# Performance work log

Hardware: AMD Instinct MI355X
Metric: run time of the kernel (lower is better)

Reference implementation:

```python
import jax, jax.numpy as jnp
import numpy as np

LEVELS = 2
_H0 = jnp.array([0.0322231, -0.01260397, -0.09921954, 0.2978578,
                 0.80373875, 0.49761867, -0.02963553, -0.07576571], dtype=jnp.float32)
_H1 = _H0[::-1] * jnp.array([-1.0, 1.0] * 4, dtype=jnp.float32)  # db4 QMF


def subband_conv2d(x, kernel_2d, stride):
    # depthwise grouped conv: same 2D kernel applied to every channel
    C = x.shape[-1]
    k = jnp.tile(kernel_2d[:, :, None, None], (1, 1, 1, C))  # HWIO with I=1, groups=C
    return jax.lax.conv_general_dilated(
        x, k, window_strides=(stride, stride), padding='SAME',
        dimension_numbers=('NHWC', 'HWIO', 'NHWC'), feature_group_count=C)


def _upsample2d(t):
    B, H, W, C = t.shape
    return jnp.zeros((B, 2 * H, 2 * W, C), t.dtype).at[:, ::2, ::2, :].set(t)


def _local_conv(t, w):
    # per-spatial-position linear map over channels: [B,H,W,I] x [I,O,W,H] -> [B,H,W,O]
    return jnp.einsum('bhwi,iowh->bhwo', t, w)


def setup_inputs() -> dict:
    key = jax.random.key(0)
    ks = jax.random.split(key, 9)
    B, H, W, C, O = 16, 128, 128, 64, 64
    inp = {
        'x': jax.random.normal(ks[0], (B, H, W, C), dtype=jnp.float32),
        'wLL': 0.02 * jax.random.normal(ks[1], (C, O, 32, 32), dtype=jnp.float32),
        'wLH_l0': 0.02 * jax.random.normal(ks[2], (C, O, 64, 64), dtype=jnp.float32),
        'wHL_l0': 0.02 * jax.random.normal(ks[3], (C, O, 64, 64), dtype=jnp.float32),
        'wHH_l0': 0.02 * jax.random.normal(ks[4], (C, O, 64, 64), dtype=jnp.float32),
        'wLH_l1': 0.02 * jax.random.normal(ks[5], (C, O, 32, 32), dtype=jnp.float32),
        'wHL_l1': 0.02 * jax.random.normal(ks[6], (C, O, 32, 32), dtype=jnp.float32),
        'wHH_l1': 0.02 * jax.random.normal(ks[7], (C, O, 32, 32), dtype=jnp.float32),
    }
    return inp


def reference(x, wLL, wLH_l0, wHL_l0, wHH_l0, wLH_l1, wHL_l1, wHH_l1):
    h0, h1 = _H0, _H1
    g0, g1 = h0[::-1], h1[::-1]
    # H=W=128 is divisible by 2**levels, so no symmetric padding is needed.
    res = x
    details = []
    for _ in range(LEVELS):
        cLL = subband_conv2d(res, jnp.outer(h0, h0), 2)
        cLH = subband_conv2d(res, jnp.outer(h0, h1), 2)
        cHL = subband_conv2d(res, jnp.outer(h1, h0), 2)
        cHH = subband_conv2d(res, jnp.outer(h1, h1), 2)
        details.append((cLH, cHL, cHH))
        res = cLL
    yA = _local_conv(res, wLL)  # [B,32,32,O]
    det_w = [(wLH_l0, wHL_l0, wHH_l0), (wLH_l1, wHL_l1, wHH_l1)]
    td = []
    for i in range(LEVELS):
        lh, hl, hh = details[i]
        wlh, whl, whh = det_w[i]
        td.append((_local_conv(lh, wlh), _local_conv(hl, whl), _local_conv(hh, whh)))
    r = yA
    for i in reversed(range(LEVELS)):
        yLH, yHL, yHH = td[i]
        r = (subband_conv2d(_upsample2d(r), jnp.outer(g0, g0), 1)
             + subband_conv2d(_upsample2d(yLH), jnp.outer(g0, g1), 1)
             + subband_conv2d(_upsample2d(yHL), jnp.outer(g1, g0), 1)
             + subband_conv2d(_upsample2d(yHH), jnp.outer(g1, g1), 1))
    return r
```

## Files before the change

kernel.cpp:

```cpp
#include <hip/hip_runtime.h>

__device__ __constant__ float H0[8] = { 0.0322231f, -0.01260397f, -0.09921954f,  0.2978578f,
                                        0.80373875f, 0.49761867f, -0.02963553f, -0.07576571f};
__device__ __constant__ float H1[8] = { 0.07576571f, -0.02963553f, -0.49761867f, 0.80373875f,
                                       -0.2978578f, -0.09921954f,  0.01260397f,  0.0322231f};
__device__ __constant__ float G0[8] = {-0.07576571f, -0.02963553f,  0.49761867f, 0.80373875f,
                                        0.2978578f,  -0.09921954f, -0.01260397f, 0.0322231f};
__device__ __constant__ float G1[8] = { 0.0322231f,   0.01260397f, -0.09921954f, -0.2978578f,
                                        0.80373875f, -0.49761867f, -0.02963553f, 0.07576571f};

template<int HIN>
__global__ __launch_bounds__(256) void fwd_dwt(const float* __restrict__ in,
                                               float* __restrict__ oLL, float* __restrict__ oLH,
                                               float* __restrict__ oHL, float* __restrict__ oHH)
{
    constexpr int OH = HIN / 2;
    constexpr int TQ = OH / 2;
    const int tid = threadIdx.x;
    const int c = tid & 63;
    const int s = blockIdx.x * 4 + (tid >> 6);
    const int j = s % TQ;
    const int i = (s / TQ) % TQ;
    const int b = s / (TQ * TQ);

    float acc[2][2][4];
#pragma unroll
    for (int a = 0; a < 2; ++a)
#pragma unroll
        for (int d = 0; d < 2; ++d)
#pragma unroll
            for (int k = 0; k < 4; ++k) acc[a][d][k] = 0.f;

    const int iw0 = 4 * j - 3;
#pragma unroll
    for (int r = 0; r < 10; ++r) {
        const int ih = 4 * i + r - 3;
        if ((unsigned)ih < (unsigned)HIN) {
            const float* row = in + ((b * HIN + ih) * HIN) * 64 + c;
            float xv[10];
#pragma unroll
            for (int v = 0; v < 10; ++v) {
                const int iw = iw0 + v;
                xv[v] = ((unsigned)iw < (unsigned)HIN) ? row[iw * 64] : 0.f;
            }
            float h00 = 0.f, h01 = 0.f, h10 = 0.f, h11 = 0.f;
#pragma unroll
            for (int v = 0; v < 8; ++v) {
                h00 += H0[v] * xv[v];
                h10 += H1[v] * xv[v];
                h01 += H0[v] * xv[v + 2];
                h11 += H1[v] * xv[v + 2];
            }
#pragma unroll
            for (int ii = 0; ii < 2; ++ii) {
                const int u = r - 2 * ii;
                if (0 <= u && u < 8) {
                    const float a0 = H0[u], a1 = H1[u];
                    acc[ii][0][0] += a0 * h00;
                    acc[ii][0][1] += a0 * h10;
                    acc[ii][0][2] += a1 * h00;
                    acc[ii][0][3] += a1 * h10;
                    acc[ii][1][0] += a0 * h01;
                    acc[ii][1][1] += a0 * h11;
                    acc[ii][1][2] += a1 * h01;
                    acc[ii][1][3] += a1 * h11;
                }
            }
        }
    }

#pragma unroll
    for (int ii = 0; ii < 2; ++ii)
#pragma unroll
        for (int jj = 0; jj < 2; ++jj) {
            const int oh = 2 * i + ii, ow = 2 * j + jj;
            const int oidx = ((b * OH + oh) * OH + ow) * 64 + c;
            oLL[oidx] = acc[ii][jj][0];
            oLH[oidx] = acc[ii][jj][1];
            oHL[oidx] = acc[ii][jj][2];
            oHH[oidx] = acc[ii][jj][3];
        }
}

template<int HD>
__global__ __launch_bounds__(256) void act_tr(const float* __restrict__ in,
                                              float* __restrict__ outp)
{
    __shared__ float Ld[64][HD + 1];
    const int w = blockIdx.x;
    const int b = blockIdx.y;
    const int t = threadIdx.x;

    {
        const int i = t & 63;
        const int hq = t >> 6;
#pragma unroll
        for (int s = 0; s < HD / 4; ++s) {
            const int h = hq * (HD / 4) + s;
            Ld[i][h] = in[((size_t)(b * HD + h) * HD + w) * 64 + i];
        }
    }
    __syncthreads();
    {
        const int h = t & (HD - 1);
        const int iq = t / HD;
        constexpr int NIQ = 256 / HD;
#pragma unroll
        for (int s = 0; s < 64 / NIQ; ++s) {
            const int i = s * NIQ + iq;
            outp[((size_t)(w * 64 + i) * 16 + b) * HD + h] = Ld[i][h];
        }
    }
}

template<int HD, int OT, int HG>
__global__ __launch_bounds__(256) void local_conv_direct(
    const float* __restrict__ a0, const float* __restrict__ a1,
    const float* __restrict__ a2, const float* __restrict__ a3,
    const float* __restrict__ w0, const float* __restrict__ w1,
    const float* __restrict__ w2, const float* __restrict__ w3,
    float* __restrict__ o0, float* __restrict__ o1,
    float* __restrict__ o2, float* __restrict__ o3)
{
    constexpr int WH  = HD * HD;
    constexpr int NOO = OT / 8;
    constexpr int NBQ = 8 / NOO;
    constexpr int NB  = 16 / NBQ;
    constexpr int NO4 = OT / 4;
    constexpr int NEX = 256 / (NO4 * 32);
    constexpr int NF  = NB / NEX;

    __shared__ float E[NB][32][33];

    const int z = blockIdx.z;
    const float* act = (z == 0) ? a0 : (z == 1) ? a1 : (z == 2) ? a2 : a3;
    const float* wgt = (z == 0) ? w0 : (z == 1) ? w1 : (z == 2) ? w2 : w3;
    float*       out = (z == 0) ? o0 : (z == 1) ? o1 : (z == 2) ? o2 : o3;

    const int bx    = blockIdx.x;
    const int hg    = bx % HG;
    const int og    = bx / HG;
    const int hbase = hg * 32;
    const int w     = blockIdx.y;
    const int t     = threadIdx.x;

    const int hc = t & 31;
    const int r  = t >> 5;
    const int oo = r & (NOO - 1);
    const int bq = r / NOO;

    const float* wp = wgt + (size_t)(og * OT + oo * 8) * WH + w * HD + hbase + hc;
    const float* ap = act + ((size_t)(w * 64) * 16 + bq * NB) * HD + hbase + hc;

    float acc[NB][8];
#pragma unroll
    for (int j = 0; j < NB; ++j)
#pragma unroll
        for (int q = 0; q < 8; ++q) acc[j][q] = 0.f;

    for (int chunk = 0; chunk < 16; ++chunk) {
        float wr[4][8];
        float ar[4][NB];
#pragma unroll
        for (int i = 0; i < 4; ++i) {
            const int ig = chunk * 4 + i;
#pragma unroll
            for (int q = 0; q < 8; ++q)
                wr[i][q] = wp[(size_t)(ig * 64 + q) * WH];
#pragma unroll
            for (int j = 0; j < NB; ++j)
                ar[i][j] = ap[(size_t)(ig * 16 + j) * HD];
        }
#pragma unroll
        for (int i = 0; i < 4; ++i)
#pragma unroll
            for (int j = 0; j < NB; ++j) {
                const float a = ar[i][j];
#pragma unroll
                for (int q = 0; q < 8; ++q)
                    acc[j][q] += a * wr[i][q];
            }
    }

    const int oF  = t & (NO4 - 1);
    const int hcF = (t / NO4) & 31;
    const int ex  = t / (NO4 * 32);

    for (int p = 0; p < NBQ; ++p) {
        if (p) __syncthreads();
        if (bq == p) {
#pragma unroll
            for (int j = 0; j < NB; ++j)
#pragma unroll
                for (int q = 0; q < 8; ++q)
                    E[j][hc][oo * 8 + q] = acc[j][q];
        }
        __syncthreads();
#pragma unroll
        for (int f = 0; f < NF; ++f) {
            const int bi = ex + f * NEX;
            float4 v = make_float4(E[bi][hcF][oF * 4 + 0], E[bi][hcF][oF * 4 + 1],
                                   E[bi][hcF][oF * 4 + 2], E[bi][hcF][oF * 4 + 3]);
            const int b = p * NB + bi;
            *(float4*)(out + ((size_t)(b * HD + hbase + hcF) * HD + w) * 64
                       + og * OT + oF * 4) = v;
        }
    }
}

template<int HOUT>
__global__ __launch_bounds__(256) void inv_dwt(const float* __restrict__ yLL,
                                               const float* __restrict__ yLH,
                                               const float* __restrict__ yHL,
                                               const float* __restrict__ yHH,
                                               float* __restrict__ out)
{
    constexpr int HS = HOUT / 2;
    const int tid = threadIdx.x;
    const int c = tid & 63;
    const int s = blockIdx.x * 4 + (tid >> 6);
    const int j = s % HS;
    const int i = (s / HS) % HS;
    const int b = s / (HS * HS);

    float Pe[4] = {0.f, 0.f, 0.f, 0.f}, Po[4] = {0.f, 0.f, 0.f, 0.f};
    float Qe[4] = {0.f, 0.f, 0.f, 0.f}, Qo[4] = {0.f, 0.f, 0.f, 0.f};

#pragma unroll
    for (int ku = 0; ku < 4; ++ku) {
        const int m = i - 1 + ku;
        if ((unsigned)m < (unsigned)HS) {
            const float a0e = G0[1 + 2 * ku], a0o = G0[2 * ku];
            const float a1e = G1[1 + 2 * ku], a1o = G1[2 * ku];
            const int rowoff = (b * HS + m) * HS;
#pragma unroll
            for (int kv = 0; kv < 4; ++kv) {
                const int n = j - 1 + kv;
                if ((unsigned)n < (unsigned)HS) {
                    const int idx = (rowoff + n) * 64 + c;
                    const float yll = yLL[idx], ylh = yLH[idx];
                    const float yhl = yHL[idx], yhh = yHH[idx];
                    Pe[kv] += a0e * yll + a1e * yhl;
                    Po[kv] += a0o * yll + a1o * yhl;
                    Qe[kv] += a0e * ylh + a1e * yhh;
                    Qo[kv] += a0o * ylh + a1o * yhh;
                }
            }
        }
    }

    float o00 = 0.f, o01 = 0.f, o10 = 0.f, o11 = 0.f;
#pragma unroll
    for (int kv = 0; kv < 4; ++kv) {
        const float b0e = G0[1 + 2 * kv], b0o = G0[2 * kv];
        const float b1e = G1[1 + 2 * kv], b1o = G1[2 * kv];
        o00 += b0e * Pe[kv] + b1e * Qe[kv];
        o01 += b0o * Pe[kv] + b1o * Qe[kv];
        o10 += b0e * Po[kv] + b1e * Qo[kv];
        o11 += b0o * Po[kv] + b1o * Qo[kv];
    }

    const int h0 = 2 * i, w0 = 2 * j;
    const int base = ((b * HOUT + h0) * HOUT + w0) * 64 + c;
    out[base] = o00;
    out[base + 64] = o01;
    out[base + HOUT * 64] = o10;
    out[base + HOUT * 64 + 64] = o11;
}

extern "C" void kernel_launch(void* const* d_in, const int* in_sizes, int n_in,
                              void* d_out, int out_size, void* d_ws, size_t ws_size,
                              hipStream_t stream)
{
    const float* x    = (const float*)d_in[0];
    const float* wLL  = (const float*)d_in[1];
    const float* wLH0 = (const float*)d_in[2];
    const float* wHL0 = (const float*)d_in[3];
    const float* wHH0 = (const float*)d_in[4];
    const float* wLH1 = (const float*)d_in[5];
    const float* wHL1 = (const float*)d_in[6];
    const float* wHH1 = (const float*)d_in[7];
    float* out = (float*)d_out;
    float* ws  = (float*)d_ws;

    const int S0 = 16 * 64 * 64 * 64;
    const int S1 = 16 * 32 * 32 * 64;

    float* c0 = out;
    float* A0 = out;
    float* A1 = out + 3 * S0;

    float* c1 = ws;
    float* t0 = ws + 4 * S1;
    float* t1 = ws + 4 * S1 + 3 * S0;
    float* yA = ws + 7 * S1 + 3 * S0;
    float* r1 = ws;

    fwd_dwt<128><<<16 * 32 * 32 / 4, 256, 0, stream>>>(x, c0, c0 + S0, c0 + 2 * S0, c0 + 3 * S0);

    fwd_dwt<64><<<16 * 16 * 16 / 4, 256, 0, stream>>>(c0,
        c1 + 0 * S1, c1 + 1 * S1, c1 + 2 * S1, c1 + 3 * S1);

    act_tr<64><<<dim3(64, 16), 256, 0, stream>>>(c0 + 1 * S0, A0 + 0 * S0);
    act_tr<64><<<dim3(64, 16), 256, 0, stream>>>(c0 + 2 * S0, A0 + 1 * S0);
    act_tr<64><<<dim3(64, 16), 256, 0, stream>>>(c0 + 3 * S0, A0 + 2 * S0);

    act_tr<32><<<dim3(32, 16), 256, 0, stream>>>(c1 + 0 * S1, A1 + 0 * S1);
    act_tr<32><<<dim3(32, 16), 256, 0, stream>>>(c1 + 1 * S1, A1 + 1 * S1);
    act_tr<32><<<dim3(32, 16), 256, 0, stream>>>(c1 + 2 * S1, A1 + 2 * S1);
    act_tr<32><<<dim3(32, 16), 256, 0, stream>>>(c1 + 3 * S1, A1 + 3 * S1);

    local_conv_direct<64, 16, 2><<<dim3(8, 64, 3), 256, 0, stream>>>(
        A0 + 0 * S0, A0 + 1 * S0, A0 + 2 * S0, nullptr,
        wLH0, wHL0, wHH0, nullptr,
        t0 + 0 * S0, t0 + 1 * S0, t0 + 2 * S0, nullptr);

    local_conv_direct<32, 16, 1><<<dim3(4, 32, 4), 256, 0, stream>>>(
        A1 + 1 * S1, A1 + 2 * S1, A1 + 3 * S1, A1 + 0 * S1,
        wLH1, wHL1, wHH1, wLL,
        t1 + 0 * S1, t1 + 1 * S1, t1 + 2 * S1, yA);

    inv_dwt<64><<<16 * 32 * 32 / 4, 256, 0, stream>>>(
        yA, t1 + 0 * S1, t1 + 1 * S1, t1 + 2 * S1, r1);

    inv_dwt<128><<<16 * 64 * 64 / 4, 256, 0, stream>>>(
        r1, t0 + 0 * S0, t0 + 1 * S0, t0 + 2 * S0, out);
}
```

Baseline: 337.2 us.

## Retile local conv with 16 outputs per thread and XCD-aware block remap

Rewrites the local-conv kernel so each thread accumulates 16 output channels over fewer batch rows, and each block covers the full H column for one w and output group. Blocks are launched on a flat 1D grid whose index is permuted across the 8 XCDs, so neighbouring blocks share weight and activation lines in the same L2. Staging in LDS now uses float4 reads from a padded tile. More accumulators per thread raise register pressure and may lower occupancy.

Result: faster. 330.3 us (-2.1%).

```diff
diff --git a/kernel.cpp b/kernel.cpp
--- a/kernel.cpp
+++ b/kernel.cpp
@@ -113,8 +113,8 @@
     }
 }
 
-template<int HD, int OT, int HG>
-__global__ __launch_bounds__(256) void local_conv_direct(
+template<int HD>
+__global__ __launch_bounds__(256) void local_conv_v7(
     const float* __restrict__ a0, const float* __restrict__ a1,
     const float* __restrict__ a2, const float* __restrict__ a3,
     const float* __restrict__ w0, const float* __restrict__ w1,
@@ -122,88 +122,87 @@
     float* __restrict__ o0, float* __restrict__ o1,
     float* __restrict__ o2, float* __restrict__ o3)
 {
-    constexpr int WH  = HD * HD;
-    constexpr int NOO = OT / 8;
-    constexpr int NBQ = 8 / NOO;
-    constexpr int NB  = 16 / NBQ;
-    constexpr int NO4 = OT / 4;
-    constexpr int NEX = 256 / (NO4 * 32);
-    constexpr int NF  = NB / NEX;
-
-    __shared__ float E[NB][32][33];
-
-    const int z = blockIdx.z;
+    constexpr int WH   = HD * HD;
+    constexpr int NR   = 256 / HD;
+    constexpr int NB   = 16 / NR;
+    constexpr int PERZ = 4 * HD;
+    constexpr int NBE  = 64 / HD;
+    constexpr int NF   = NB / NBE;
+
+    __shared__ float E[NB][HD][20];
+
+    const int nwg = gridDim.x;
+    const int hb  = blockIdx.x;
+    const int l   = (hb & 7) * (nwg >> 3) + (hb >> 3);
+
+    const int z   = l / PERZ;
+    const int rem = l - z * PERZ;
+    const int w   = rem >> 2;
+    const int og  = rem & 3;
+
     const float* act = (z == 0) ? a0 : (z == 1) ? a1 : (z == 2) ? a2 : a3;
     const float* wgt = (z == 0) ? w0 : (z == 1) ? w1 : (z == 2) ? w2 : w3;
     float*       out = (z == 0) ? o0 : (z == 1) ? o1 : (z == 2) ? o2 : o3;
 
-    const int bx    = blockIdx.x;
-    const int hg    = bx % HG;
-    const int og    = bx / HG;
-    const int hbase = hg * 32;
-    const int w     = blockIdx.y;
-    const int t     = threadIdx.x;
-
-    const int hc = t & 31;
-    const int r  = t >> 5;
-    const int oo = r & (NOO - 1);
-    const int bq = r / NOO;
-
-    const float* wp = wgt + (size_t)(og * OT + oo * 8) * WH + w * HD + hbase + hc;
-    const float* ap = act + ((size_t)(w * 64) * 16 + bq * NB) * HD + hbase + hc;
-
-    float acc[NB][8];
+    const int t  = threadIdx.x;
+    const int hc = t & (HD - 1);
+    const int r  = t / HD;
+    const int b0 = r * NB;
+
+    const float* wp = wgt + (size_t)(og * 16) * WH + w * HD + hc;
+    const float* ap = act + ((size_t)(w * 64) * 16 + b0) * HD + hc;
+
+    float acc[NB][16];
 #pragma unroll
     for (int j = 0; j < NB; ++j)
 #pragma unroll
-        for (int q = 0; q < 8; ++q) acc[j][q] = 0.f;
-
-    for (int chunk = 0; chunk < 16; ++chunk) {
-        float wr[4][8];
-        float ar[4][NB];
-#pragma unroll
-        for (int i = 0; i < 4; ++i) {
-            const int ig = chunk * 4 + i;
-#pragma unroll
-            for (int q = 0; q < 8; ++q)
-                wr[i][q] = wp[(size_t)(ig * 64 + q) * WH];
+        for (int q = 0; q < 16; ++q) acc[j][q] = 0.f;
+
+    for (int ch = 0; ch < 32; ++ch) {
+        const int i0 = ch * 2;
+        float wr[2][16];
+        float ar[2][NB];
+#pragma unroll
+        for (int ii = 0; ii < 2; ++ii) {
+#pragma unroll
+            for (int q = 0; q < 16; ++q)
+                wr[ii][q] = wp[(size_t)((i0 + ii) * 64 + q) * WH];
 #pragma unroll
             for (int j = 0; j < NB; ++j)
-                ar[i][j] = ap[(size_t)(ig * 16 + j) * HD];
-        }
-#pragma unroll
-        for (int i = 0; i < 4; ++i)
+                ar[ii][j] = ap[(size_t)((i0 + ii) * 16 + j) * HD];
+        }
+#pragma unroll
+        for (int ii = 0; ii < 2; ++ii)
 #pragma unroll
             for (int j = 0; j < NB; ++j) {
-                const float a = ar[i][j];
-#pragma unroll
-                for (int q = 0; q < 8; ++q)
-                    acc[j][q] += a * wr[i][q];
-            }
-    }
-
-    const int oF  = t & (NO4 - 1);
-    const int hcF = (t / NO4) & 31;
-    const int ex  = t / (NO4 * 32);
-
-    for (int p = 0; p < NBQ; ++p) {
+                const float a = ar[ii][j];
+#pragma unroll
+                for (int q = 0; q < 16; ++q)
+                    acc[j][q] += a * wr[ii][q];
+            }
+    }
+
+    const int oF = t & 3;
+    const int h2 = (t >> 2) & (HD - 1);
+    const int be = t / (4 * HD);
+
+    for (int p = 0; p < NR; ++p) {
         if (p) __syncthreads();
-        if (bq == p) {
+        if (r == p) {
 #pragma unroll
             for (int j = 0; j < NB; ++j)
 #pragma unroll
-                for (int q = 0; q < 8; ++q)
-                    E[j][hc][oo * 8 + q] = acc[j][q];
+                for (int q = 0; q < 16; ++q)
+                    E[j][hc][q] = acc[j][q];
         }
         __syncthreads();
 #pragma unroll
         for (int f = 0; f < NF; ++f) {
-            const int bi = ex + f * NEX;
-            float4 v = make_float4(E[bi][hcF][oF * 4 + 0], E[bi][hcF][oF * 4 + 1],
-                                   E[bi][hcF][oF * 4 + 2], E[bi][hcF][oF * 4 + 3]);
+            const int bi = be + f * NBE;
+            float4 v = *(const float4*)&E[bi][h2][oF * 4];
             const int b = p * NB + bi;
-            *(float4*)(out + ((size_t)(b * HD + hbase + hcF) * HD + w) * 64
-                       + og * OT + oF * 4) = v;
+            *(float4*)(out + ((size_t)(b * HD + h2) * HD + w) * 64
+                       + og * 16 + oF * 4) = v;
         }
     }
 }
@@ -310,12 +309,12 @@
     act_tr<32><<<dim3(32, 16), 256, 0, stream>>>(c1 + 2 * S1, A1 + 2 * S1);
     act_tr<32><<<dim3(32, 16), 256, 0, stream>>>(c1 + 3 * S1, A1 + 3 * S1);
 
-    local_conv_direct<64, 16, 2><<<dim3(8, 64, 3), 256, 0, stream>>>(
+    local_conv_v7<64><<<768, 256, 0, stream>>>(
         A0 + 0 * S0, A0 + 1 * S0, A0 + 2 * S0, nullptr,
         wLH0, wHL0, wHH0, nullptr,
         t0 + 0 * S0, t0 + 1 * S0, t0 + 2 * S0, nullptr);
 
-    local_conv_direct<32, 16, 1><<<dim3(4, 32, 4), 256, 0, stream>>>(
+    local_conv_v7<32><<<512, 256, 0, stream>>>(
         A1 + 1 * S1, A1 + 2 * S1, A1 + 3 * S1, A1 + 0 * S1,
         wLH1, wHL1, wHH1, wLL,
         t1 + 0 * S1, t1 + 1 * S1, t1 + 2 * S1, yA);
```
